# Kernel tuning notes

Measured on AMD Instinct MI355X. Metric: run time of the kernel, lower is better.

The kernel has to match this reference:

```python
import jax, jax.numpy as jnp
import numpy as np
from jax import lax

D_MODEL, D_STATE, D_CONV, EXPAND = 1024, 16, 4, 2
D_INNER = D_MODEL * EXPAND
LN_EPS = 1e-5


def _silu(v):
    return v * jax.nn.sigmoid(v)


def setup_inputs() -> dict:
    key = jax.random.key(0)
    ks = jax.random.split(key, 12)
    B, T = 4, 2048
    x = jax.random.normal(ks[0], (B, T, D_MODEL), dtype=jnp.float32)
    W_in = jax.random.normal(ks[1], (2 * D_INNER, D_MODEL), dtype=jnp.float32) * (D_MODEL ** -0.5)
    conv_w = jax.random.normal(ks[2], (D_INNER, 1, D_CONV), dtype=jnp.float32) * (D_CONV ** -0.5)
    conv_b = jax.random.normal(ks[3], (D_INNER,), dtype=jnp.float32) * 0.01
    W_x = jax.random.normal(ks[4], (2 * D_STATE, D_INNER), dtype=jnp.float32) * (D_INNER ** -0.5)
    dt_init_std = D_INNER ** -0.5
    W_dt = jax.random.uniform(ks[5], (D_INNER, D_INNER), minval=-dt_init_std, maxval=dt_init_std, dtype=jnp.float32)
    # bias = inverse softplus of dt sampled log-uniform in [dt_min, dt_max]
    dt = jnp.exp(jax.random.uniform(ks[6], (D_INNER,)) * (np.log(0.1) - np.log(0.001)) + np.log(0.001))
    b_dt = dt + jnp.log(-jnp.expm1(-dt))
    A_log = jnp.log(jnp.arange(1, D_STATE + 1, dtype=jnp.float32) * 0.5)
    D_param = jnp.ones((D_INNER,), dtype=jnp.float32)
    W_out = jax.random.normal(ks[7], (D_MODEL, D_INNER), dtype=jnp.float32) * (D_MODEL ** -0.5)
    ln_g = jnp.ones((D_INNER,), dtype=jnp.float32)
    ln_b = jnp.zeros((D_INNER,), dtype=jnp.float32)
    return {"x": x, "W_in": W_in, "conv_w": conv_w, "conv_b": conv_b, "W_x": W_x,
            "W_dt": W_dt, "b_dt": b_dt, "A_log": A_log, "D_param": D_param,
            "W_out": W_out, "ln_g": ln_g, "ln_b": ln_b}


def _forward(x, W_in, conv_w, conv_b, W_x, W_dt, b_dt, A_log, D_param, W_out, ln_g, ln_b):
    B, T, _ = x.shape
    xz = jnp.einsum('btd,ed->bte', x, W_in)            # (B,T,2*d_inner)
    xp, z = xz[..., :D_INNER], xz[..., D_INNER:]
    # depthwise causal conv1d (left pad d_conv-1, keep first T outputs)
    xc = lax.conv_general_dilated(
        jnp.transpose(xp, (0, 2, 1)), conv_w,
        window_strides=(1,), padding=[(D_CONV - 1, 0)],
        feature_group_count=D_INNER,
        dimension_numbers=('NCH', 'OIH', 'NCH')) + conv_b[None, :, None]
    xc = _silu(jnp.transpose(xc, (0, 2, 1)))           # (B,T,d_inner)
    ssm = jnp.einsum('bti,si->bts', xc, W_x)           # (B,T,2*d_state)
    Bp, Cp = ssm[..., :D_STATE], ssm[..., D_STATE:]
    dt = jax.nn.softplus(jnp.einsum('bti,oi->bto', xc, W_dt) + b_dt)
    A = -jnp.exp(A_log)                                # (d_state,)

    def step(h, inp):
        x_t, b_t, c_t, dt_t = inp                      # (B,d),(B,s),(B,s),(B,d)
        dA = jnp.exp(dt_t[..., None] * A)              # (B,d_inner,d_state)
        h = dA * h + (dt_t[..., None] * b_t[:, None, :]) * x_t[..., None]
        y_t = jnp.einsum('bds,bs->bd', h, c_t)
        return h, y_t

    h0 = jnp.zeros((B, D_INNER, D_STATE), dtype=x.dtype)
    tm = lambda a: jnp.moveaxis(a, 1, 0)               # time-major
    _, ys = lax.scan(step, h0, (tm(xc), tm(Bp), tm(Cp), tm(dt)))
    y = jnp.moveaxis(ys, 0, 1)                         # (B,T,d_inner)

    mu = jnp.mean(y, axis=-1, keepdims=True)
    var = jnp.mean((y - mu) ** 2, axis=-1, keepdims=True)
    y = (y - mu) * lax.rsqrt(var + LN_EPS) * ln_g + ln_b
    y = y + xc * D_param
    y = y * _silu(z)
    return jnp.einsum('bti,di->btd', y, W_out)         # dropout is identity (eval)


def reference(x, W_in, conv_w, conv_b, W_x, W_dt, b_dt, A_log, D_param, W_out, ln_g, ln_b):
    return _forward(x, W_in, conv_w, conv_b, W_x, W_dt, b_dt, A_log, D_param, W_out, ln_g, ln_b)
```

## Files before the change

### kernel.cpp

```cpp
#include <hip/hip_runtime.h>
#include <hip/hip_bf16.h>
#include <math.h>
#include <stdint.h>

#define B_SZ 4
#define T_SZ 2048
#define DM   1024
#define DI   2048
#define DS   16
#define BT   (B_SZ*T_SZ)
#define NC   2176

typedef __attribute__((ext_vector_type(8))) short short8;
typedef __attribute__((ext_vector_type(4))) float f32x4;

__device__ __forceinline__ float siluf(float v) { return v / (1.f + __expf(-v)); }
__device__ __forceinline__ float softplusf(float x) {
    return fmaxf(x, 0.f) + log1pf(__expf(-fabsf(x)));
}
__device__ __forceinline__ unsigned short f2b(float f) {
    __hip_bfloat16 h = __float2bfloat16(f);
    return *reinterpret_cast<unsigned short*>(&h);
}
__device__ __forceinline__ float b2f(unsigned short u) {
    unsigned v = (unsigned)u << 16;
    float f;
    __builtin_memcpy(&f, &v, 4);
    return f;
}
__device__ __forceinline__ void gld_lds16(const void* g, void* l) {
    __builtin_amdgcn_global_load_lds(
        (const __attribute__((address_space(1))) unsigned int*)g,
        (__attribute__((address_space(3))) unsigned int*)l,
        16, 0, 0);
}

__global__ __launch_bounds__(256)
void cvt_bf16(const float* __restrict__ src, unsigned short* __restrict__ dst, int n4)
{
    int i = blockIdx.x * 256 + threadIdx.x;
    if (i >= n4) return;
    float4 v = ((const float4*)src)[i];
    ushort4 o;
    o.x = f2b(v.x); o.y = f2b(v.y); o.z = f2b(v.z); o.w = f2b(v.w);
    ((ushort4*)dst)[i] = o;
}

__global__ __launch_bounds__(256)
void cvt_wc(const float* __restrict__ Wdt, const float* __restrict__ Wx,
            unsigned short* __restrict__ dst)
{
    const int n4 = NC * (DI / 4);
    int i = blockIdx.x * 256 + threadIdx.x;
    if (i >= n4) return;
    int row = i >> 9;
    int c4  = i & 511;
    float4 v;
    if (row < 2048)      v = ((const float4*)Wdt)[(size_t)row * 512 + c4];
    else if (row < 2080) v = ((const float4*)Wx)[(size_t)(row - 2048) * 512 + c4];
    else                 v = make_float4(0.f, 0.f, 0.f, 0.f);
    ushort4 o;
    o.x = f2b(v.x); o.y = f2b(v.y); o.z = f2b(v.z); o.w = f2b(v.w);
    ((ushort4*)dst)[i] = o;
}

__global__ __launch_bounds__(256)
void gemm_mfma(const unsigned short* __restrict__ A,
               const unsigned short* __restrict__ Bm,
               int M, int N, int K, int mode,
               const float* __restrict__ bias,
               void* __restrict__ o0, void* __restrict__ o1, void* __restrict__ o2)
{
    __shared__ unsigned short As[2][128 * 32];
    __shared__ unsigned short Bs[2][128 * 32];

    const int npn = N >> 7;
    const int pid = blockIdx.x;
    const int gsz = 16 * npn;
    const int gid = pid / gsz;
    const int pm  = gid * 16 + (pid % 16);
    const int pn  = (pid % gsz) / 16;
    const int bm  = pm * 128;
    const int bn  = pn * 128;

    const int tid  = threadIdx.x;
    const int lane = tid & 63;
    const int wave = tid >> 6;
    const int wm   = (wave >> 1) * 64;
    const int wn   = (wave & 1) * 64;

    f32x4 zero4 = {0.f, 0.f, 0.f, 0.f};
    f32x4 acc[4][4];
#pragma unroll
    for (int i = 0; i < 4; i++)
#pragma unroll
        for (int j = 0; j < 4; j++) acc[i][j] = zero4;

    const int sr = tid >> 2;
    const int sc = (tid & 3) * 8;
    const unsigned short* Ag = A  + (size_t)(bm + sr) * K + sc;
    const unsigned short* Bg = Bm + (size_t)(bn + sr) * K + sc;

    const int fr = lane & 15;
    const int fk = (lane >> 4) * 8;

    for (int k0 = 0; k0 < K; k0 += 64) {
#pragma unroll
        for (int kh = 0; kh < 2; kh++) {
            const int ko = k0 + kh * 32;
            gld_lds16(Ag + ko,                  &As[kh][tid * 8]);
            gld_lds16(Ag + (size_t)64 * K + ko, &As[kh][2048 + tid * 8]);
            gld_lds16(Bg + ko,                  &Bs[kh][tid * 8]);
            gld_lds16(Bg + (size_t)64 * K + ko, &Bs[kh][2048 + tid * 8]);
        }
        __syncthreads();
#pragma unroll
        for (int kh = 0; kh < 2; kh++) {
            short8 af[4], bf[4];
#pragma unroll
            for (int i = 0; i < 4; i++) {
                af[i] = *(const short8*)&As[kh][(wm + i * 16 + fr) * 32 + fk];
                bf[i] = *(const short8*)&Bs[kh][(wn + i * 16 + fr) * 32 + fk];
            }
#pragma unroll
            for (int i = 0; i < 4; i++)
#pragma unroll
                for (int j = 0; j < 4; j++)
                    acc[i][j] = __builtin_amdgcn_mfma_f32_16x16x32_bf16(
                        af[i], bf[j], acc[i][j], 0, 0, 0);
        }
        __syncthreads();
    }

    const int cr0 = bm + wm + (lane >> 4) * 4;
    const int cc0 = bn + wn + (lane & 15);
#pragma unroll
    for (int i = 0; i < 4; i++) {
#pragma unroll
        for (int j = 0; j < 4; j++) {
            const int col = cc0 + j * 16;
#pragma unroll
            for (int r = 0; r < 4; r++) {
                const int row = cr0 + i * 16 + r;
                float v = acc[i][j][r];
                if (mode == 0) {
                    if (col < 2048)
                        ((unsigned short*)o0)[(size_t)row * 2048 + col] = f2b(v);
                    else
                        ((unsigned short*)o1)[(size_t)row * 2048 + col - 2048] = f2b(v);
                } else if (mode == 1) {
                    if (col < 2048) {
                        ((float*)o0)[(size_t)row * 2048 + col] = softplusf(v + bias[col]);
                    } else if (col < 2064) {
                        ((float*)o1)[(size_t)row * DS + (col - 2048)] = v;
                    } else if (col < 2080) {
                        ((float*)o2)[(size_t)row * DS + (col - 2064)] = v;
                    }
                } else {
                    ((float*)o0)[(size_t)row * N + col] = v;
                }
            }
        }
    }
}

__global__ __launch_bounds__(256)
void conv_silu(const unsigned short* __restrict__ xpb, const float* __restrict__ cw,
               const float* __restrict__ cb, unsigned short* __restrict__ xcb)
{
    const int idx = blockIdx.x * 256 + threadIdx.x;
    const int i  = idx & (DI - 1);
    const int bt = idx >> 11;
    const int t  = bt & (T_SZ - 1);
    float acc = cb[i];
    float4 w = *(const float4*)(cw + (size_t)i * 4);
    float wr[4] = {w.x, w.y, w.z, w.w};
#pragma unroll
    for (int k = 0; k < 4; k++) {
        const int tt = t - 3 + k;
        if (tt >= 0)
            acc = fmaf(b2f(xpb[(size_t)(bt - 3 + k) * DI + i]), wr[k], acc);
    }
    xcb[idx] = f2b(siluf(acc));
}

#define CH 16
#define CL (T_SZ / CH)

__global__ __launch_bounds__(256)
void scan2(const unsigned short* __restrict__ xcb, float* __restrict__ dty,
           const float* __restrict__ Bp, const float* __restrict__ Cp,
           const float* __restrict__ A_log)
{
    __shared__ float shH[CH][16][DS];
    __shared__ float shP[CH][16][DS];
    __shared__ float shI[CH][16][DS];
    const int tid = threadIdx.x;
    const int c = tid >> 4;
    const int g = tid & 15;
    const int b = blockIdx.y;
    const int d = blockIdx.x * 16 + g;

    float A[DS];
#pragma unroll
    for (int s = 0; s < DS; s++) A[s] = -__expf(A_log[s]);

    const size_t colbase = (size_t)b * T_SZ * DI + d;
    const unsigned short* xp = xcb + colbase + (size_t)c * CL * DI;
    float* dp = dty + colbase + (size_t)c * CL * DI;
    const float4* Bb = (const float4*)(Bp + ((size_t)b * T_SZ + c * CL) * DS);
    const float4* Cb = (const float4*)(Cp + ((size_t)b * T_SZ + c * CL) * DS);

    float h[DS], P[DS];
#pragma unroll
    for (int s = 0; s < DS; s++) { h[s] = 0.f; P[s] = 1.f; }

    for (int i = 0; i < CL; i++) {
        const float xv = b2f(xp[(size_t)i * DI]);
        const float dv = dp[(size_t)i * DI];
        float4 Bv[4] = {Bb[i*4+0], Bb[i*4+1], Bb[i*4+2], Bb[i*4+3]};
        const float* bs = (const float*)&Bv[0];
        const float dx = dv * xv;
#pragma unroll
        for (int s = 0; s < DS; s++) {
            const float dA = __expf(dv * A[s]);
            h[s] = fmaf(dA, h[s], dx * bs[s]);
            P[s] *= dA;
        }
    }
#pragma unroll
    for (int s = 0; s < DS; s += 4) {
        *(float4*)&shH[c][g][s] = make_float4(h[s], h[s+1], h[s+2], h[s+3]);
        *(float4*)&shP[c][g][s] = make_float4(P[s], P[s+1], P[s+2], P[s+3]);
    }
    __syncthreads();

    {
        const int g2 = tid >> 4, s2 = tid & 15;
        float hin = 0.f;
        shI[0][g2][s2] = 0.f;
        for (int cc = 1; cc < CH; cc++) {
            hin = fmaf(shP[cc-1][g2][s2], hin, shH[cc-1][g2][s2]);
            shI[cc][g2][s2] = hin;
        }
    }
    __syncthreads();

#pragma unroll
    for (int s = 0; s < DS; s++) h[s] = shI[c][g][s];
    for (int i = 0; i < CL; i++) {
        const float xv = b2f(xp[(size_t)i * DI]);
        const float dv = dp[(size_t)i * DI];
        float4 Bv[4] = {Bb[i*4+0], Bb[i*4+1], Bb[i*4+2], Bb[i*4+3]};
        float4 Cv[4] = {Cb[i*4+0], Cb[i*4+1], Cb[i*4+2], Cb[i*4+3]};
        const float* bs = (const float*)&Bv[0];
        const float* cs = (const float*)&Cv[0];
        const float dx = dv * xv;
        float yv = 0.f;
#pragma unroll
        for (int s = 0; s < DS; s++) {
            const float dA = __expf(dv * A[s]);
            h[s] = fmaf(dA, h[s], dx * bs[s]);
            yv = fmaf(h[s], cs[s], yv);
        }
        dp[(size_t)i * DI] = yv;
    }
}

__global__ __launch_bounds__(256)
void ln_fuse(const float* __restrict__ y, const unsigned short* __restrict__ xcb,
             const unsigned short* __restrict__ zb, const float* __restrict__ g,
             const float* __restrict__ bln, const float* __restrict__ Dp,
             unsigned short* __restrict__ yb)
{
    __shared__ float rs[256], rss[256];
    const int bt  = blockIdx.x;
    const int tid = threadIdx.x;
    const float* yr = y + (size_t)bt * DI;
    const unsigned short* xr = xcb + (size_t)bt * DI;
    const unsigned short* zr = zb + (size_t)bt * DI;
    unsigned short* orow = yb + (size_t)bt * DI;

    float v[8];
    float s = 0.f, ss = 0.f;
#pragma unroll
    for (int j = 0; j < 8; j++) {
        v[j] = yr[tid + j * 256];
        s  += v[j];
        ss += v[j] * v[j];
    }
    rs[tid] = s; rss[tid] = ss;
    __syncthreads();
    for (int off = 128; off > 0; off >>= 1) {
        if (tid < off) { rs[tid] += rs[tid + off]; rss[tid] += rss[tid + off]; }
        __syncthreads();
    }
    const float mu   = rs[0] * (1.f / DI);
    const float var  = rss[0] * (1.f / DI) - mu * mu;
    const float rstd = rsqrtf(var + 1e-5f);
#pragma unroll
    for (int j = 0; j < 8; j++) {
        const int dcol = tid + j * 256;
        float yn = (v[j] - mu) * rstd * g[dcol] + bln[dcol];
        yn += b2f(xr[dcol]) * Dp[dcol];
        yn *= siluf(b2f(zr[dcol]));
        orow[dcol] = f2b(yn);
    }
}

extern "C" void kernel_launch(void* const* d_in, const int* in_sizes, int n_in,
                              void* d_out, int out_size, void* d_ws, size_t ws_size,
                              hipStream_t stream)
{
    const float* x      = (const float*)d_in[0];
    const float* W_in   = (const float*)d_in[1];
    const float* conv_w = (const float*)d_in[2];
    const float* conv_b = (const float*)d_in[3];
    const float* W_x    = (const float*)d_in[4];
    const float* W_dt   = (const float*)d_in[5];
    const float* b_dt   = (const float*)d_in[6];
    const float* A_log  = (const float*)d_in[7];
    const float* D_par  = (const float*)d_in[8];
    const float* W_out  = (const float*)d_in[9];
    const float* ln_g   = (const float*)d_in[10];
    const float* ln_b   = (const float*)d_in[11];
    float* out = (float*)d_out;

    char* w = (char*)d_ws;
    const size_t MB = 1ull << 20;
    unsigned short* xpb    = (unsigned short*)(w);
    unsigned short* zb     = (unsigned short*)(w + 32 * MB);
    unsigned short* xcb    = (unsigned short*)(w + 64 * MB);
    float*          dts    = (float*)(w + 96 * MB);
    unsigned short* xb     = (unsigned short*)(w + 96 * MB);
    unsigned short* W_inb  = (unsigned short*)(w + 112 * MB);
    unsigned short* Wcb    = (unsigned short*)(w + 160 * MB);
    unsigned short* W_outb = (unsigned short*)(w + 169 * MB);
    float*          BpF    = (float*)(w + 174 * MB);
    float*          CpF    = BpF + (size_t)BT * DS;
    unsigned short* yb     = xpb;

    dim3 blk(256);

    cvt_bf16<<<dim3((BT * DM / 4 + 255) / 256), blk, 0, stream>>>(x, xb, BT * DM / 4);
    cvt_bf16<<<dim3((2 * DI * DM / 4 + 255) / 256), blk, 0, stream>>>(W_in, W_inb, 2 * DI * DM / 4);
    cvt_wc<<<dim3((NC * DI / 4 + 255) / 256), blk, 0, stream>>>(W_dt, W_x, Wcb);
    cvt_bf16<<<dim3((DM * DI / 4 + 255) / 256), blk, 0, stream>>>(W_out, W_outb, DM * DI / 4);

    gemm_mfma<<<dim3((BT / 128) * (2 * DI / 128)), blk, 0, stream>>>(
        xb, W_inb, BT, 2 * DI, DM, 0, nullptr, xpb, zb, nullptr);

    conv_silu<<<dim3(BT * DI / 256), blk, 0, stream>>>(xpb, conv_w, conv_b, xcb);

    gemm_mfma<<<dim3((BT / 128) * (NC / 128)), blk, 0, stream>>>(
        xcb, Wcb, BT, NC, DI, 1, b_dt, dts, BpF, CpF);

    scan2<<<dim3(DI / 16, B_SZ), blk, 0, stream>>>(xcb, dts, BpF, CpF, A_log);

    ln_fuse<<<dim3(BT), blk, 0, stream>>>(dts, xcb, zb, ln_g, ln_b, D_par, yb);

    gemm_mfma<<<dim3((BT / 128) * (DM / 128)), blk, 0, stream>>>(
        yb, W_outb, BT, DM, DI, 2, nullptr, out, nullptr, nullptr);
}
```

Baseline: 737.4 us.

## Use 512-thread GEMM blocks with double-buffered K=32 LDS prefetch

The MFMA GEMM goes from 256 to 512 threads. Each of the 8 waves now computes a 64x32 sub-tile instead of 64x64, halving accumulator registers per wave. The K loop now steps by 32 with a ping-pong LDS buffer, so the next slice is loaded while the current one is computed, replacing the load-all-then-compute pattern. This adds latency hiding and more waves per CU, at the cost of a barrier every 32 K and smaller per-wave MFMA reuse.

```diff
diff --git a/kernel.cpp b/kernel.cpp
--- a/kernel.cpp
+++ b/kernel.cpp
@@ -64,7 +64,7 @@
     ((ushort4*)dst)[i] = o;
 }
 
-__global__ __launch_bounds__(256)
+__global__ __launch_bounds__(512)
 void gemm_mfma(const unsigned short* __restrict__ A,
                const unsigned short* __restrict__ Bm,
                int M, int N, int K, int mode,
@@ -86,15 +86,15 @@
     const int tid  = threadIdx.x;
     const int lane = tid & 63;
     const int wave = tid >> 6;
-    const int wm   = (wave >> 1) * 64;
-    const int wn   = (wave & 1) * 64;
+    const int wm   = (wave >> 2) * 64;
+    const int wn   = (wave & 3) * 32;
 
     f32x4 zero4 = {0.f, 0.f, 0.f, 0.f};
-    f32x4 acc[4][4];
+    f32x4 acc[4][2];
 #pragma unroll
     for (int i = 0; i < 4; i++)
 #pragma unroll
-        for (int j = 0; j < 4; j++) acc[i][j] = zero4;
+        for (int j = 0; j < 2; j++) acc[i][j] = zero4;
 
     const int sr = tid >> 2;
     const int sc = (tid & 3) * 8;
@@ -104,32 +104,31 @@
     const int fr = lane & 15;
     const int fk = (lane >> 4) * 8;
 
-    for (int k0 = 0; k0 < K; k0 += 64) {
-#pragma unroll
-        for (int kh = 0; kh < 2; kh++) {
-            const int ko = k0 + kh * 32;
-            gld_lds16(Ag + ko,                  &As[kh][tid * 8]);
-            gld_lds16(Ag + (size_t)64 * K + ko, &As[kh][2048 + tid * 8]);
-            gld_lds16(Bg + ko,                  &Bs[kh][tid * 8]);
-            gld_lds16(Bg + (size_t)64 * K + ko, &Bs[kh][2048 + tid * 8]);
-        }
+    gld_lds16(Ag, &As[0][tid * 8]);
+    gld_lds16(Bg, &Bs[0][tid * 8]);
+    __syncthreads();
+
+    int cur = 0;
+    for (int k0 = 0; k0 < K; k0 += 32) {
+        if (k0 + 32 < K) {
+            gld_lds16(Ag + k0 + 32, &As[cur ^ 1][tid * 8]);
+            gld_lds16(Bg + k0 + 32, &Bs[cur ^ 1][tid * 8]);
+        }
+        short8 af[4], bf[2];
+#pragma unroll
+        for (int i = 0; i < 4; i++)
+            af[i] = *(const short8*)&As[cur][(wm + i * 16 + fr) * 32 + fk];
+#pragma unroll
+        for (int j = 0; j < 2; j++)
+            bf[j] = *(const short8*)&Bs[cur][(wn + j * 16 + fr) * 32 + fk];
+#pragma unroll
+        for (int i = 0; i < 4; i++)
+#pragma unroll
+            for (int j = 0; j < 2; j++)
+                acc[i][j] = __builtin_amdgcn_mfma_f32_16x16x32_bf16(
+                    af[i], bf[j], acc[i][j], 0, 0, 0);
         __syncthreads();
-#pragma unroll
-        for (int kh = 0; kh < 2; kh++) {
-            short8 af[4], bf[4];
-#pragma unroll
-            for (int i = 0; i < 4; i++) {
-                af[i] = *(const short8*)&As[kh][(wm + i * 16 + fr) * 32 + fk];
-                bf[i] = *(const short8*)&Bs[kh][(wn + i * 16 + fr) * 32 + fk];
-            }
-#pragma unroll
-            for (int i = 0; i < 4; i++)
-#pragma unroll
-                for (int j = 0; j < 4; j++)
-                    acc[i][j] = __builtin_amdgcn_mfma_f32_16x16x32_bf16(
-                        af[i], bf[j], acc[i][j], 0, 0, 0);
-        }
-        __syncthreads();
+        cur ^= 1;
     }
 
     const int cr0 = bm + wm + (lane >> 4) * 4;
@@ -137,7 +136,7 @@
 #pragma unroll
     for (int i = 0; i < 4; i++) {
 #pragma unroll
-        for (int j = 0; j < 4; j++) {
+        for (int j = 0; j < 2; j++) {
             const int col = cc0 + j * 16;
 #pragma unroll
             for (int r = 0; r < 4; r++) {
@@ -341,24 +340,25 @@
     unsigned short* yb     = xpb;
 
     dim3 blk(256);
+    dim3 blk512(512);
 
     cvt_bf16<<<dim3((BT * DM / 4 + 255) / 256), blk, 0, stream>>>(x, xb, BT * DM / 4);
     cvt_bf16<<<dim3((2 * DI * DM / 4 + 255) / 256), blk, 0, stream>>>(W_in, W_inb, 2 * DI * DM / 4);
     cvt_wc<<<dim3((NC * DI / 4 + 255) / 256), blk, 0, stream>>>(W_dt, W_x, Wcb);
     cvt_bf16<<<dim3((DM * DI / 4 + 255) / 256), blk, 0, stream>>>(W_out, W_outb, DM * DI / 4);
 
-    gemm_mfma<<<dim3((BT / 128) * (2 * DI / 128)), blk, 0, stream>>>(
+    gemm_mfma<<<dim3((BT / 128) * (2 * DI / 128)), blk512, 0, stream>>>(
         xb, W_inb, BT, 2 * DI, DM, 0, nullptr, xpb, zb, nullptr);
 
     conv_silu<<<dim3(BT * DI / 256), blk, 0, stream>>>(xpb, conv_w, conv_b, xcb);
 
-    gemm_mfma<<<dim3((BT / 128) * (NC / 128)), blk, 0, stream>>>(
+    gemm_mfma<<<dim3((BT / 128) * (NC / 128)), blk512, 0, stream>>>(
         xcb, Wcb, BT, NC, DI, 1, b_dt, dts, BpF, CpF);
 
     scan2<<<dim3(DI / 16, B_SZ), blk, 0, stream>>>(xcb, dts, BpF, CpF, A_log);
 
     ln_fuse<<<dim3(BT), blk, 0, stream>>>(dts, xcb, zb, ln_g, ln_b, D_par, yb);
 
-    gemm_mfma<<<dim3((BT / 128) * (DM / 128)), blk, 0, stream>>>(
+    gemm_mfma<<<dim3((BT / 128) * (DM / 128)), blk512, 0, stream>>>(
         yb, W_outb, BT, DM, DI, 2, nullptr, out, nullptr, nullptr);
 }
```

Result: faster. 633.1 us (-14.1%).

## Load GEMM MFMA fragments directly from global memory with register double-buffering

Applied to the files above, without the earlier changes.

The shared-memory staging (global_load_lds into LDS tiles plus two barriers per K step) is replaced by per-wave direct global loads of the MFMA fragments into registers, with a ping-pong prefetch of the next 32-wide K slice while the current one is multiplied. Launch bounds now request 3 blocks per SM. This removes LDS traffic and block-level synchronisation. The cost is that each wave reloads A/B rows that other waves in the block share, doubling global/L2 traffic, and uses uncoalesced 16-byte row-strided loads with higher register pressure.

```diff
diff --git a/kernel.cpp b/kernel.cpp
--- a/kernel.cpp
+++ b/kernel.cpp
@@ -27,12 +27,6 @@
     float f;
     __builtin_memcpy(&f, &v, 4);
     return f;
-}
-__device__ __forceinline__ void gld_lds16(const void* g, void* l) {
-    __builtin_amdgcn_global_load_lds(
-        (const __attribute__((address_space(1))) unsigned int*)g,
-        (__attribute__((address_space(3))) unsigned int*)l,
-        16, 0, 0);
 }
 
 __global__ __launch_bounds__(256)
@@ -64,16 +58,13 @@
     ((ushort4*)dst)[i] = o;
 }
 
-__global__ __launch_bounds__(256)
+__global__ __launch_bounds__(256, 3)
 void gemm_mfma(const unsigned short* __restrict__ A,
                const unsigned short* __restrict__ Bm,
                int M, int N, int K, int mode,
                const float* __restrict__ bias,
                void* __restrict__ o0, void* __restrict__ o1, void* __restrict__ o2)
 {
-    __shared__ unsigned short As[2][128 * 32];
-    __shared__ unsigned short Bs[2][128 * 32];
-
     const int npn = N >> 7;
     const int pid = blockIdx.x;
     const int gsz = 16 * npn;
@@ -88,6 +79,12 @@
     const int wave = tid >> 6;
     const int wm   = (wave >> 1) * 64;
     const int wn   = (wave & 1) * 64;
+    const int fr   = lane & 15;
+    const int fk   = (lane >> 4) * 8;
+
+    const unsigned short* Ap = A  + (size_t)(bm + wm + fr) * K + fk;
+    const unsigned short* Bp = Bm + (size_t)(bn + wn + fr) * K + fk;
+    const size_t r16 = (size_t)16 * K;
 
     f32x4 zero4 = {0.f, 0.f, 0.f, 0.f};
     f32x4 acc[4][4];
@@ -96,40 +93,38 @@
 #pragma unroll
         for (int j = 0; j < 4; j++) acc[i][j] = zero4;
 
-    const int sr = tid >> 2;
-    const int sc = (tid & 3) * 8;
-    const unsigned short* Ag = A  + (size_t)(bm + sr) * K + sc;
-    const unsigned short* Bg = Bm + (size_t)(bn + sr) * K + sc;
-
-    const int fr = lane & 15;
-    const int fk = (lane >> 4) * 8;
+    short8 a0[4], b0[4], a1[4], b1[4];
+#pragma unroll
+    for (int i = 0; i < 4; i++) {
+        a0[i] = *(const short8*)(Ap + i * r16);
+        b0[i] = *(const short8*)(Bp + i * r16);
+    }
 
     for (int k0 = 0; k0 < K; k0 += 64) {
 #pragma unroll
-        for (int kh = 0; kh < 2; kh++) {
-            const int ko = k0 + kh * 32;
-            gld_lds16(Ag + ko,                  &As[kh][tid * 8]);
-            gld_lds16(Ag + (size_t)64 * K + ko, &As[kh][2048 + tid * 8]);
-            gld_lds16(Bg + ko,                  &Bs[kh][tid * 8]);
-            gld_lds16(Bg + (size_t)64 * K + ko, &Bs[kh][2048 + tid * 8]);
-        }
-        __syncthreads();
-#pragma unroll
-        for (int kh = 0; kh < 2; kh++) {
-            short8 af[4], bf[4];
+        for (int i = 0; i < 4; i++) {
+            a1[i] = *(const short8*)(Ap + i * r16 + k0 + 32);
+            b1[i] = *(const short8*)(Bp + i * r16 + k0 + 32);
+        }
+#pragma unroll
+        for (int i = 0; i < 4; i++)
+#pragma unroll
+            for (int j = 0; j < 4; j++)
+                acc[i][j] = __builtin_amdgcn_mfma_f32_16x16x32_bf16(
+                    a0[i], b0[j], acc[i][j], 0, 0, 0);
+        if (k0 + 64 < K) {
 #pragma unroll
             for (int i = 0; i < 4; i++) {
-                af[i] = *(const short8*)&As[kh][(wm + i * 16 + fr) * 32 + fk];
-                bf[i] = *(const short8*)&Bs[kh][(wn + i * 16 + fr) * 32 + fk];
+                a0[i] = *(const short8*)(Ap + i * r16 + k0 + 64);
+                b0[i] = *(const short8*)(Bp + i * r16 + k0 + 64);
             }
-#pragma unroll
-            for (int i = 0; i < 4; i++)
-#pragma unroll
-                for (int j = 0; j < 4; j++)
-                    acc[i][j] = __builtin_amdgcn_mfma_f32_16x16x32_bf16(
-                        af[i], bf[j], acc[i][j], 0, 0, 0);
-        }
-        __syncthreads();
+        }
+#pragma unroll
+        for (int i = 0; i < 4; i++)
+#pragma unroll
+            for (int j = 0; j < 4; j++)
+                acc[i][j] = __builtin_amdgcn_mfma_f32_16x16x32_bf16(
+                    a1[i], b1[j], acc[i][j], 0, 0, 0);
     }
 
     const int cr0 = bm + wm + (lane >> 4) * 4;
```

Result: slower. 1.052 ms (+42.7%).

## Use 256x128 GEMM tiles with 8 waves, LDS swizzle and double-buffered prefetch

Applied to the files above, without the earlier changes.

The MFMA GEMM now uses 512-thread blocks computing 256x128 output tiles, which halves the grid and reuses each B tile across twice as many rows. The loop switches to a 32-wide K step with ping-pong LDS buffers, so the next tile is prefetched while MFMAs run on the current one, and there is one barrier per step. LDS rows are XOR-swizzled to reduce bank conflicts on the fragment reads. The cost is fewer blocks per launch, which may leave CUs underused on the smaller GEMMs, and higher per-block LDS and register use.

```diff
diff --git a/kernel.cpp b/kernel.cpp
--- a/kernel.cpp
+++ b/kernel.cpp
@@ -64,14 +64,14 @@
     ((ushort4*)dst)[i] = o;
 }
 
-__global__ __launch_bounds__(256)
+__global__ __launch_bounds__(512)
 void gemm_mfma(const unsigned short* __restrict__ A,
                const unsigned short* __restrict__ Bm,
                int M, int N, int K, int mode,
                const float* __restrict__ bias,
                void* __restrict__ o0, void* __restrict__ o1, void* __restrict__ o2)
 {
-    __shared__ unsigned short As[2][128 * 32];
+    __shared__ unsigned short As[2][256 * 32];
     __shared__ unsigned short Bs[2][128 * 32];
 
     const int npn = N >> 7;
@@ -80,7 +80,7 @@
     const int gid = pid / gsz;
     const int pm  = gid * 16 + (pid % 16);
     const int pn  = (pid % gsz) / 16;
-    const int bm  = pm * 128;
+    const int bm  = pm * 256;
     const int bn  = pn * 128;
 
     const int tid  = threadIdx.x;
@@ -88,6 +88,8 @@
     const int wave = tid >> 6;
     const int wm   = (wave >> 1) * 64;
     const int wn   = (wave & 1) * 64;
+    const int fr   = lane & 15;
+    const int fj   = lane >> 4;
 
     f32x4 zero4 = {0.f, 0.f, 0.f, 0.f};
     f32x4 acc[4][4];
@@ -96,40 +98,55 @@
 #pragma unroll
         for (int j = 0; j < 4; j++) acc[i][j] = zero4;
 
-    const int sr = tid >> 2;
-    const int sc = (tid & 3) * 8;
-    const unsigned short* Ag = A  + (size_t)(bm + sr) * K + sc;
-    const unsigned short* Bg = Bm + (size_t)(bn + sr) * K + sc;
-
-    const int fr = lane & 15;
-    const int fk = (lane >> 4) * 8;
-
-    for (int k0 = 0; k0 < K; k0 += 64) {
-#pragma unroll
-        for (int kh = 0; kh < 2; kh++) {
-            const int ko = k0 + kh * 32;
-            gld_lds16(Ag + ko,                  &As[kh][tid * 8]);
-            gld_lds16(Ag + (size_t)64 * K + ko, &As[kh][2048 + tid * 8]);
-            gld_lds16(Bg + ko,                  &Bs[kh][tid * 8]);
-            gld_lds16(Bg + (size_t)64 * K + ko, &Bs[kh][2048 + tid * 8]);
-        }
+    const unsigned short* AgP[2];
+#pragma unroll
+    for (int q = 0; q < 2; q++) {
+        const int slot = q * 512 + tid;
+        const int row  = slot >> 2;
+        const int j    = (slot & 3) ^ ((row >> 1) & 3);
+        AgP[q] = A + (size_t)(bm + row) * K + j * 8;
+    }
+    const int rowB = tid >> 2;
+    const int jB   = (tid & 3) ^ ((rowB >> 1) & 3);
+    const unsigned short* BgP = Bm + (size_t)(bn + rowB) * K + jB * 8;
+
+    int aoff[4], boff[4];
+#pragma unroll
+    for (int i = 0; i < 4; i++) {
+        const int r = wm + i * 16 + fr;
+        aoff[i] = r * 32 + ((fj ^ ((r >> 1) & 3)) * 8);
+    }
+#pragma unroll
+    for (int j = 0; j < 4; j++) {
+        const int r = wn + j * 16 + fr;
+        boff[j] = r * 32 + ((fj ^ ((r >> 1) & 3)) * 8);
+    }
+
+    gld_lds16(AgP[0], &As[0][tid * 8]);
+    gld_lds16(AgP[1], &As[0][(512 + tid) * 8]);
+    gld_lds16(BgP,    &Bs[0][tid * 8]);
+    __syncthreads();
+
+    int cur = 0;
+    for (int k0 = 0; k0 < K; k0 += 32) {
+        if (k0 + 32 < K) {
+            gld_lds16(AgP[0] + k0 + 32, &As[cur ^ 1][tid * 8]);
+            gld_lds16(AgP[1] + k0 + 32, &As[cur ^ 1][(512 + tid) * 8]);
+            gld_lds16(BgP    + k0 + 32, &Bs[cur ^ 1][tid * 8]);
+        }
+        short8 af[4], bf[4];
+#pragma unroll
+        for (int i = 0; i < 4; i++) af[i] = *(const short8*)&As[cur][aoff[i]];
+#pragma unroll
+        for (int j = 0; j < 4; j++) bf[j] = *(const short8*)&Bs[cur][boff[j]];
+#pragma unroll
+        for (int i = 0; i < 4; i++)
+#pragma unroll
+            for (int j = 0; j < 4; j++)
+                acc[i][j] = __builtin_amdgcn_mfma_f32_16x16x32_bf16(
+                    af[i], bf[j], acc[i][j], 0, 0, 0);
         __syncthreads();
-#pragma unroll
-        for (int kh = 0; kh < 2; kh++) {
-            short8 af[4], bf[4];
-#pragma unroll
-            for (int i = 0; i < 4; i++) {
-                af[i] = *(const short8*)&As[kh][(wm + i * 16 + fr) * 32 + fk];
-                bf[i] = *(const short8*)&Bs[kh][(wn + i * 16 + fr) * 32 + fk];
-            }
-#pragma unroll
-            for (int i = 0; i < 4; i++)
-#pragma unroll
-                for (int j = 0; j < 4; j++)
-                    acc[i][j] = __builtin_amdgcn_mfma_f32_16x16x32_bf16(
-                        af[i], bf[j], acc[i][j], 0, 0, 0);
-        }
-        __syncthreads();
+        cur ^= 1;
     }
 
     const int cr0 = bm + wm + (lane >> 4) * 4;
@@ -341,24 +358,25 @@
     unsigned short* yb     = xpb;
 
     dim3 blk(256);
+    dim3 blk512(512);
 
     cvt_bf16<<<dim3((BT * DM / 4 + 255) / 256), blk, 0, stream>>>(x, xb, BT * DM / 4);
     cvt_bf16<<<dim3((2 * DI * DM / 4 + 255) / 256), blk, 0, stream>>>(W_in, W_inb, 2 * DI * DM / 4);
     cvt_wc<<<dim3((NC * DI / 4 + 255) / 256), blk, 0, stream>>>(W_dt, W_x, Wcb);
     cvt_bf16<<<dim3((DM * DI / 4 + 255) / 256), blk, 0, stream>>>(W_out, W_outb, DM * DI / 4);
 
-    gemm_mfma<<<dim3((BT / 128) * (2 * DI / 128)), blk, 0, stream>>>(
+    gemm_mfma<<<dim3((BT / 256) * (2 * DI / 128)), blk512, 0, stream>>>(
         xb, W_inb, BT, 2 * DI, DM, 0, nullptr, xpb, zb, nullptr);
 
     conv_silu<<<dim3(BT * DI / 256), blk, 0, stream>>>(xpb, conv_w, conv_b, xcb);
 
-    gemm_mfma<<<dim3((BT / 128) * (NC / 128)), blk, 0, stream>>>(
+    gemm_mfma<<<dim3((BT / 256) * (NC / 128)), blk512, 0, stream>>>(
         xcb, Wcb, BT, NC, DI, 1, b_dt, dts, BpF, CpF);
 
     scan2<<<dim3(DI / 16, B_SZ), blk, 0, stream>>>(xcb, dts, BpF, CpF, A_log);
 
     ln_fuse<<<dim3(BT), blk, 0, stream>>>(dts, xcb, zb, ln_g, ln_b, D_par, yb);
 
-    gemm_mfma<<<dim3((BT / 128) * (DM / 128)), blk, 0, stream>>>(
+    gemm_mfma<<<dim3((BT / 256) * (DM / 128)), blk512, 0, stream>>>(
         yb, W_outb, BT, DM, DI, 2, nullptr, out, nullptr, nullptr);
 }
```

New measurement: 700.7 us. 5.0% less time.
